# Kernel optimization log

Hardware: AMD Instinct MI355X
Metric: run time of the kernel (lower is better)

## Reference

```python
import jax, jax.numpy as jnp
import numpy as np

EMBED_DIM = 1024
HEADS = 16
HEAD_DIM = EMBED_DIM // HEADS


def setup_inputs() -> dict:
    key = jax.random.key(0)
    ks = jax.random.split(key, 5)
    B, N, C = 2, 2048, EMBED_DIM
    scale = 1.0 / np.sqrt(C)
    x = jax.random.normal(ks[0], (B, N, C), dtype=jnp.float32)
    W_qkv = jax.random.normal(ks[1], (C, 3 * C), dtype=jnp.float32) * scale
    b_qkv = jax.random.normal(ks[2], (3 * C,), dtype=jnp.float32) * 0.01
    W_out = jax.random.normal(ks[3], (C, C), dtype=jnp.float32) * scale
    b_out = jax.random.normal(ks[4], (C,), dtype=jnp.float32) * 0.01
    return {"x": x, "W_qkv": W_qkv, "b_qkv": b_qkv, "W_out": W_out, "b_out": b_out}


def reference(x, W_qkv, b_qkv, W_out, b_out):
    B, N, C = x.shape
    qkv = x @ W_qkv + b_qkv                      # [B, N, 3C]
    qkv = qkv.reshape(B, N, 3, HEADS, HEAD_DIM)
    qkv = jnp.transpose(qkv, (2, 0, 3, 1, 4))    # [3, B, H, N, d]
    q, k, v = qkv[0], qkv[1], qkv[2]
    attn = jnp.einsum('bhnd,bhmd->bhnm', q, k) / np.sqrt(HEAD_DIM)
    attn = jax.nn.softmax(attn, axis=-1)
    out = jnp.einsum('bhnm,bhmd->bhnd', attn, v)  # [B, H, N, d]
    out = jnp.transpose(out, (0, 2, 1, 3)).reshape(B, N, C)
    return out @ W_out + b_out
```

## Files before the change

kernel.cpp:

```cpp
#include <hip/hip_runtime.h>
#include <stdint.h>

typedef __bf16 bf16_t;
typedef bf16_t bf16x8 __attribute__((ext_vector_type(8)));
typedef bf16_t bf16x2v __attribute__((ext_vector_type(2)));
typedef short short4v __attribute__((ext_vector_type(4)));
typedef float f32x4 __attribute__((ext_vector_type(4)));
typedef uint32_t u32x2 __attribute__((ext_vector_type(2)));

#define BATCH 2
#define SEQ 2048
#define CDIM 1024
#define NH 16
#define HD 64

#define QSCALE 0.18033688011f

__device__ __forceinline__ uint16_t f32_bf16(float f) {
    __bf16 h = (__bf16)f;
    return __builtin_bit_cast(uint16_t, h);
}

__device__ __forceinline__ uint32_t pack_bf16(float a, float b) {
    bf16x2v t;
    t.x = (__bf16)a;
    t.y = (__bf16)b;
    return __builtin_bit_cast(uint32_t, t);
}

__device__ __forceinline__ bf16x8 ld8(const uint16_t* p) {
    return *reinterpret_cast<const bf16x8*>(p);
}

__device__ __forceinline__ void gld16(const uint16_t* g, uint16_t* l) {
    __builtin_amdgcn_global_load_lds(
        (__attribute__((address_space(1))) void*)(g),
        (__attribute__((address_space(3))) void*)(l), 16, 0, 0);
}

#define LDS_FENCE() asm volatile("s_waitcnt lgkmcnt(0)" ::: "memory")

__global__ __launch_bounds__(256) void prep_kernel(
        const float* __restrict__ x, uint16_t* __restrict__ x_bf,
        const float* __restrict__ Wqkv, uint16_t* __restrict__ wqkvT,
        const float* __restrict__ Wout, uint16_t* __restrict__ woutT) {
    const int bid = blockIdx.x, tid = threadIdx.x;
    if (bid < 4096) {
        int i = (bid * 256 + tid) * 4;
        float4 v = *(const float4*)(x + i);
        ushort4 o;
        o.x = f32_bf16(v.x);
        o.y = f32_bf16(v.y);
        o.z = f32_bf16(v.z);
        o.w = f32_bf16(v.w);
        *(ushort4*)(x_bf + i) = o;
        return;
    }
    __shared__ float tile[32][33];
    const float* in;
    uint16_t* outp;
    int idx, Cc, ncx;
    if (bid < 4096 + 3072) { idx = bid - 4096; in = Wqkv; outp = wqkvT; Cc = 3072; ncx = 96; }
    else                   { idx = bid - 7168; in = Wout; outp = woutT; Cc = 1024; ncx = 32; }
    const int R = 1024;
    int bx = idx % ncx, by = idx / ncx;
    int c0 = bx * 32, r0 = by * 32;
    int tx = tid & 31, ty = tid >> 5;
#pragma unroll
    for (int i = 0; i < 4; i++)
        tile[ty + i * 8][tx] = in[(size_t)(r0 + ty + i * 8) * Cc + c0 + tx];
    __syncthreads();
#pragma unroll
    for (int i = 0; i < 4; i++) {
        int rr = ty + i * 8;
        outp[(size_t)(c0 + rr) * R + r0 + tx] = f32_bf16(tile[tx][rr]);
    }
}

template <int BM, int BN, int MODE>
__global__ __launch_bounds__(256) void gemm_t(
        const uint16_t* __restrict__ A, const uint16_t* __restrict__ Bt, int K,
        const float* __restrict__ bias,
        uint16_t* __restrict__ qw, uint16_t* __restrict__ kw, uint16_t* __restrict__ vt,
        float* __restrict__ out) {
    constexpr int WT_M = BM / 2, WT_N = BN / 2;
    constexpr int MI = WT_M / 16, NJ = WT_N / 16;
    constexpr int ASEG_W = BM / 64, BSEG_W = BN / 64;
    constexpr int AB = 2 * BM * 32 + 2 * BN * 32;
    constexpr int TS = (MODE == 0) ? 4 * 64 * 68 : 0;
    constexpr int SM = AB > TS ? AB : TS;
    __shared__ uint16_t smem[SM];
    uint16_t* As = smem;
    uint16_t* Bs = smem + 2 * BM * 32;

    const int m0 = blockIdx.y * BM, n0 = blockIdx.x * BN;
    const int tid = threadIdx.x;
    const int w = tid >> 6, lane = tid & 63;
    const int quad = lane >> 4, l16 = lane & 15;
    const int wm = (w >> 1) * WT_M, wn = (w & 1) * WT_N;

    const int srow = lane >> 2;
    const int schunk = (lane & 3) ^ (srow & 3);

    const uint16_t* aP[ASEG_W];
    const uint16_t* bP[BSEG_W];
    int aL[ASEG_W], bL[BSEG_W];
#pragma unroll
    for (int s = 0; s < ASEG_W; s++) {
        int seg = w * ASEG_W + s;
        aP[s] = A + (size_t)(m0 + seg * 16 + srow) * K + schunk * 8;
        aL[s] = seg * 512;
    }
#pragma unroll
    for (int s = 0; s < BSEG_W; s++) {
        int seg = w * BSEG_W + s;
        bP[s] = Bt + (size_t)(n0 + seg * 16 + srow) * K + schunk * 8;
        bL[s] = seg * 512;
    }

    auto stage = [&](int buf, int k0) {
#pragma unroll
        for (int s = 0; s < ASEG_W; s++) gld16(aP[s] + k0, As + buf * BM * 32 + aL[s]);
#pragma unroll
        for (int s = 0; s < BSEG_W; s++) gld16(bP[s] + k0, Bs + buf * BN * 32 + bL[s]);
    };

    const int cslot = (quad ^ (l16 & 3)) * 8;
    f32x4 acc[MI][NJ] = {};

    stage(0, 0);
    const int iters = K / 32;
    for (int it = 0; it < iters; ++it) {
        __syncthreads();
        if (it + 1 < iters) stage((it + 1) & 1, (it + 1) * 32);
        const uint16_t* A_ = As + (it & 1) * BM * 32;
        const uint16_t* B_ = Bs + (it & 1) * BN * 32;
        bf16x8 af[MI], bfr[NJ];
#pragma unroll
        for (int i = 0; i < MI; i++) af[i] = ld8(&A_[(wm + i * 16 + l16) * 32 + cslot]);
#pragma unroll
        for (int j = 0; j < NJ; j++) bfr[j] = ld8(&B_[(wn + j * 16 + l16) * 32 + cslot]);
#pragma unroll
        for (int i = 0; i < MI; i++)
#pragma unroll
            for (int j = 0; j < NJ; j++)
                acc[i][j] = __builtin_amdgcn_mfma_f32_16x16x32_bf16(af[i], bfr[j], acc[i][j], 0, 0, 0);
    }

    const int nbase = n0 + wn;
    float bj[NJ];
#pragma unroll
    for (int j = 0; j < NJ; j++) bj[j] = bias[nbase + j * 16 + l16];

    if constexpr (MODE == 1) {
#pragma unroll
        for (int j = 0; j < NJ; j++) {
#pragma unroll
            for (int i = 0; i < MI; i++)
#pragma unroll
                for (int r = 0; r < 4; r++) {
                    int m = m0 + wm + i * 16 + quad * 4 + r;
                    out[(size_t)m * CDIM + nbase + j * 16 + l16] = acc[i][j][r] + bj[j];
                }
        }
    } else {
        __syncthreads();
        uint16_t* T = smem + w * 64 * 68;
        const int gmb = m0 + wm;
        const int b = gmb >> 11, ns0 = gmb & 2047;

        if (nbase < 2048) {
            const int which = nbase >> 10, h = (nbase & 1023) >> 6;
            const float sc = (which == 0) ? QSCALE : 1.0f;
#pragma unroll
            for (int i = 0; i < 4; i++)
#pragma unroll
                for (int j = 0; j < 4; j++)
#pragma unroll
                    for (int r = 0; r < 4; r++)
                        T[(i * 16 + quad * 4 + r) * 68 + j * 16 + l16] =
                            f32_bf16((acc[i][j][r] + bj[j]) * sc);
            LDS_FENCE();
            uint16_t* dst = ((which == 0) ? qw : kw) +
                            (((size_t)b * NH + h) * SEQ + ns0 + lane) * HD;
#pragma unroll
            for (int g = 0; g < 8; g++) {
                bf16x8 v = ld8(&T[lane * 68 + g * 8]);
                *(bf16x8*)(dst + g * 8) = v;
            }
        } else {
#pragma unroll
            for (int i = 0; i < 4; i++)
#pragma unroll
                for (int j = 0; j < 4; j++) {
                    u32x2 pr;
                    pr.x = pack_bf16(acc[i][j][0] + bj[j], acc[i][j][1] + bj[j]);
                    pr.y = pack_bf16(acc[i][j][2] + bj[j], acc[i][j][3] + bj[j]);
                    *(u32x2*)&T[(j * 16 + l16) * 68 + i * 16 + quad * 4] = pr;
                }
            LDS_FENCE();
            const int h = (nbase - 2048) >> 6;
            uint16_t* dst = vt + (((size_t)b * NH + h) * HD + lane) * SEQ + ns0;
#pragma unroll
            for (int g = 0; g < 16; g++) {
                u32x2 d2 = *(const u32x2*)&T[lane * 68 + g * 4];
                int npos = (g & 3) * 16 + (g >> 2) * 4;
                *(u32x2*)(dst + npos) = d2;
            }
        }
    }
}

__global__ __launch_bounds__(256) void attn_kernel(
        const uint16_t* __restrict__ qg, const uint16_t* __restrict__ kg,
        const uint16_t* __restrict__ vt, uint16_t* __restrict__ og) {
    __shared__ uint16_t Ks[2][64 * 64];
    __shared__ uint16_t Vs[2][64 * 64];

    const int bh = blockIdx.x;
    const int qt = blockIdx.y;
    const int tid = threadIdx.x;
    const int w = tid >> 6, lane = tid & 63;
    const int quad = lane >> 4, l16 = lane & 15;
    const int qrow0 = qt * 128 + w * 32;
    const size_t base = (size_t)bh * SEQ * HD;

    bf16x8 qf[2][2];
#pragma unroll
    for (int mg = 0; mg < 2; mg++)
#pragma unroll
        for (int ks = 0; ks < 2; ks++)
            qf[mg][ks] = ld8(qg + base + (size_t)(qrow0 + mg * 16 + l16) * HD + ks * 32 + quad * 8);

    const int srow = lane >> 3;
    const int schunk = (lane & 7) ^ srow;
    const int seg0 = w * 2, seg1 = seg0 + 1;
    const uint16_t* ksrc0 = kg + base + (size_t)(seg0 * 8 + srow) * HD + schunk * 8;
    const uint16_t* ksrc1 = kg + base + (size_t)(seg1 * 8 + srow) * HD + schunk * 8;
    const uint16_t* vsrc0 = vt + base + (size_t)(seg0 * 8 + srow) * SEQ + schunk * 8;
    const uint16_t* vsrc1 = vt + base + (size_t)(seg1 * 8 + srow) * SEQ + schunk * 8;
    const int soff0 = seg0 * 512, soff1 = seg1 * 512;

    f32x4 o_acc[2][4] = {};
    f32x4 l_acc[2] = {};
    const short4v ones = { (short)0x3F80, (short)0x3F80, (short)0x3F80, (short)0x3F80 };

    gld16(ksrc0, &Ks[0][soff0]); gld16(ksrc1, &Ks[0][soff1]);
    gld16(vsrc0, &Vs[0][soff0]); gld16(vsrc1, &Vs[0][soff1]);
    ksrc0 += 64 * HD; ksrc1 += 64 * HD; vsrc0 += 64; vsrc1 += 64;

    for (int it = 0; it < SEQ / 64; ++it) {
        __syncthreads();
        if (it + 1 < SEQ / 64) {
            int pb = (it + 1) & 1;
            gld16(ksrc0, &Ks[pb][soff0]); gld16(ksrc1, &Ks[pb][soff1]);
            gld16(vsrc0, &Vs[pb][soff0]); gld16(vsrc1, &Vs[pb][soff1]);
            ksrc0 += 64 * HD; ksrc1 += 64 * HD; vsrc0 += 64; vsrc1 += 64;
        }
        const uint16_t* K_ = Ks[it & 1];
        const uint16_t* V_ = Vs[it & 1];

        f32x4 S[2][4] = {};
#pragma unroll
        for (int nf = 0; nf < 4; nf++) {
#pragma unroll
            for (int ks = 0; ks < 2; ks++) {
                bf16x8 kf = ld8(&K_[(nf * 16 + l16) * 64 + (((ks * 4 + quad) ^ (l16 & 7)) * 8)]);
#pragma unroll
                for (int mg = 0; mg < 2; mg++)
                    S[mg][nf] = __builtin_amdgcn_mfma_f32_16x16x32_bf16(kf, qf[mg][ks], S[mg][nf], 0, 0, 0);
            }
        }

        uint32_t pk[2][4][2];
#pragma unroll
        for (int mg = 0; mg < 2; mg++)
#pragma unroll
            for (int nf = 0; nf < 4; nf++) {
                float p0 = __builtin_amdgcn_exp2f(S[mg][nf][0]);
                float p1 = __builtin_amdgcn_exp2f(S[mg][nf][1]);
                float p2 = __builtin_amdgcn_exp2f(S[mg][nf][2]);
                float p3 = __builtin_amdgcn_exp2f(S[mg][nf][3]);
                pk[mg][nf][0] = pack_bf16(p0, p1);
                pk[mg][nf][1] = pack_bf16(p2, p3);
            }

#pragma unroll
        for (int mg = 0; mg < 2; mg++)
#pragma unroll
            for (int kc = 0; kc < 4; kc++) {
                short4v pfrag = __builtin_bit_cast(short4v, (u32x2){pk[mg][kc][0], pk[mg][kc][1]});
                l_acc[mg] = __builtin_amdgcn_mfma_f32_16x16x16bf16_1k(ones, pfrag, l_acc[mg], 0, 0, 0);
            }

#pragma unroll
        for (int mf = 0; mf < 4; mf++) {
            const int ro = (mf * 16 + l16) * 64;
            uint4 v0 = *(const uint4*)&V_[ro + (((quad * 2 + 0) ^ (l16 & 7)) * 8)];
            uint4 v1 = *(const uint4*)&V_[ro + (((quad * 2 + 1) ^ (l16 & 7)) * 8)];
            short4v vf[4];
            vf[0] = __builtin_bit_cast(short4v, (u32x2){v0.x, v0.y});
            vf[1] = __builtin_bit_cast(short4v, (u32x2){v0.z, v0.w});
            vf[2] = __builtin_bit_cast(short4v, (u32x2){v1.x, v1.y});
            vf[3] = __builtin_bit_cast(short4v, (u32x2){v1.z, v1.w});
#pragma unroll
            for (int kc = 0; kc < 4; kc++)
#pragma unroll
                for (int mg = 0; mg < 2; mg++) {
                    short4v pfrag = __builtin_bit_cast(short4v, (u32x2){pk[mg][kc][0], pk[mg][kc][1]});
                    o_acc[mg][mf] = __builtin_amdgcn_mfma_f32_16x16x16bf16_1k(vf[kc], pfrag, o_acc[mg][mf], 0, 0, 0);
                }
        }
    }

    const int b = bh >> 4, h = bh & 15;
#pragma unroll
    for (int mg = 0; mg < 2; mg++) {
        const float inv = __builtin_amdgcn_rcpf(l_acc[mg][0]);
        const int ns = qrow0 + mg * 16 + l16;
        uint16_t* orow = og + (((size_t)b * SEQ + ns) * NH + h) * HD + quad * 4;
#pragma unroll
        for (int mf = 0; mf < 4; mf++) {
            ushort4 o;
            o.x = f32_bf16(o_acc[mg][mf][0] * inv);
            o.y = f32_bf16(o_acc[mg][mf][1] * inv);
            o.z = f32_bf16(o_acc[mg][mf][2] * inv);
            o.w = f32_bf16(o_acc[mg][mf][3] * inv);
            *(ushort4*)(orow + mf * 16) = o;
        }
    }
}

extern "C" void kernel_launch(void* const* d_in, const int* in_sizes, int n_in,
                              void* d_out, int out_size, void* d_ws, size_t ws_size,
                              hipStream_t stream) {
    const float* x = (const float*)d_in[0];
    const float* Wqkv = (const float*)d_in[1];
    const float* bqkv = (const float*)d_in[2];
    const float* Wout = (const float*)d_in[3];
    const float* bout = (const float*)d_in[4];
    float* out = (float*)d_out;

    uint16_t* ws = (uint16_t*)d_ws;
    uint16_t* x_bf  = ws;
    uint16_t* wqkvT = x_bf + 4194304;
    uint16_t* woutT = wqkvT + 3145728;
    uint16_t* qw    = woutT + 1048576;
    uint16_t* kw    = qw + 4194304;
    uint16_t* vtw   = kw + 4194304;
    uint16_t* attn  = vtw + 4194304;

    prep_kernel<<<8192, 256, 0, stream>>>(x, x_bf, Wqkv, wqkvT, Wout, woutT);

    gemm_t<128, 128, 0><<<dim3(24, 32), 256, 0, stream>>>(
        x_bf, wqkvT, 1024, bqkv, qw, kw, vtw, nullptr);

    attn_kernel<<<dim3(32, 16), 256, 0, stream>>>(qw, kw, vtw, attn);

    gemm_t<64, 128, 1><<<dim3(8, 64), 256, 0, stream>>>(
        attn, woutT, 1024, bout, nullptr, nullptr, nullptr, out);
}
```

Before: 189.8 us.

## Load K/V fragments directly from global memory, drop LDS staging and MFMA row-sum

Removes the shared-memory double buffers and __syncthreads in the attention kernel, so each wave reads its K and V MFMA fragments straight from global memory (relying on L1/L2 for reuse across the four waves). The loop processes 128 keys per iteration in two 64-key sub-steps, and V loads are issued ahead of the QK MFMAs. The softmax denominator is now accumulated with scalar adds and reduced with cross-lane shuffles at the end, replacing the ones-vector MFMA. This drops block-level synchronisation and LDS traffic but adds redundant global/cache loads per wave and more register pressure.

```diff
diff --git a/kernel.cpp b/kernel.cpp
--- a/kernel.cpp
+++ b/kernel.cpp
@@ -214,9 +214,6 @@
 __global__ __launch_bounds__(256) void attn_kernel(
         const uint16_t* __restrict__ qg, const uint16_t* __restrict__ kg,
         const uint16_t* __restrict__ vt, uint16_t* __restrict__ og) {
-    __shared__ uint16_t Ks[2][64 * 64];
-    __shared__ uint16_t Vs[2][64 * 64];
-
     const int bh = blockIdx.x;
     const int qt = blockIdx.y;
     const int tid = threadIdx.x;
@@ -232,91 +229,82 @@
         for (int ks = 0; ks < 2; ks++)
             qf[mg][ks] = ld8(qg + base + (size_t)(qrow0 + mg * 16 + l16) * HD + ks * 32 + quad * 8);
 
-    const int srow = lane >> 3;
-    const int schunk = (lane & 7) ^ srow;
-    const int seg0 = w * 2, seg1 = seg0 + 1;
-    const uint16_t* ksrc0 = kg + base + (size_t)(seg0 * 8 + srow) * HD + schunk * 8;
-    const uint16_t* ksrc1 = kg + base + (size_t)(seg1 * 8 + srow) * HD + schunk * 8;
-    const uint16_t* vsrc0 = vt + base + (size_t)(seg0 * 8 + srow) * SEQ + schunk * 8;
-    const uint16_t* vsrc1 = vt + base + (size_t)(seg1 * 8 + srow) * SEQ + schunk * 8;
-    const int soff0 = seg0 * 512, soff1 = seg1 * 512;
+    const uint16_t* kp = kg + base + (size_t)l16 * HD + quad * 8;
+    const uint16_t* vp[4];
+#pragma unroll
+    for (int mf = 0; mf < 4; mf++)
+        vp[mf] = vt + base + (size_t)(mf * 16 + l16) * SEQ + quad * 16;
 
     f32x4 o_acc[2][4] = {};
-    f32x4 l_acc[2] = {};
-    const short4v ones = { (short)0x3F80, (short)0x3F80, (short)0x3F80, (short)0x3F80 };
-
-    gld16(ksrc0, &Ks[0][soff0]); gld16(ksrc1, &Ks[0][soff1]);
-    gld16(vsrc0, &Vs[0][soff0]); gld16(vsrc1, &Vs[0][soff1]);
-    ksrc0 += 64 * HD; ksrc1 += 64 * HD; vsrc0 += 64; vsrc1 += 64;
-
-    for (int it = 0; it < SEQ / 64; ++it) {
-        __syncthreads();
-        if (it + 1 < SEQ / 64) {
-            int pb = (it + 1) & 1;
-            gld16(ksrc0, &Ks[pb][soff0]); gld16(ksrc1, &Ks[pb][soff1]);
-            gld16(vsrc0, &Vs[pb][soff0]); gld16(vsrc1, &Vs[pb][soff1]);
-            ksrc0 += 64 * HD; ksrc1 += 64 * HD; vsrc0 += 64; vsrc1 += 64;
+    float l_run[2] = {0.f, 0.f};
+
+    for (int it = 0; it < SEQ / 128; ++it) {
+#pragma unroll
+        for (int sub = 0; sub < 2; sub++) {
+            uint4 v0[4], v1[4];
+#pragma unroll
+            for (int mf = 0; mf < 4; mf++) {
+                v0[mf] = *(const uint4*)(vp[mf] + sub * 64);
+                v1[mf] = *(const uint4*)(vp[mf] + sub * 64 + 8);
+            }
+
+            f32x4 S[2][4] = {};
+#pragma unroll
+            for (int nf = 0; nf < 4; nf++) {
+#pragma unroll
+                for (int ks = 0; ks < 2; ks++) {
+                    bf16x8 kf = ld8(kp + (size_t)(sub * 64 + nf * 16) * HD + ks * 32);
+#pragma unroll
+                    for (int mg = 0; mg < 2; mg++)
+                        S[mg][nf] = __builtin_amdgcn_mfma_f32_16x16x32_bf16(kf, qf[mg][ks], S[mg][nf], 0, 0, 0);
+                }
+            }
+
+            uint32_t pk[2][4][2];
+#pragma unroll
+            for (int mg = 0; mg < 2; mg++) {
+                float rs = 0.f;
+#pragma unroll
+                for (int nf = 0; nf < 4; nf++) {
+                    float p0 = __builtin_amdgcn_exp2f(S[mg][nf][0]);
+                    float p1 = __builtin_amdgcn_exp2f(S[mg][nf][1]);
+                    float p2 = __builtin_amdgcn_exp2f(S[mg][nf][2]);
+                    float p3 = __builtin_amdgcn_exp2f(S[mg][nf][3]);
+                    rs += (p0 + p1) + (p2 + p3);
+                    pk[mg][nf][0] = pack_bf16(p0, p1);
+                    pk[mg][nf][1] = pack_bf16(p2, p3);
+                }
+                l_run[mg] += rs;
+            }
+
+#pragma unroll
+            for (int mf = 0; mf < 4; mf++) {
+                short4v vf[4];
+                vf[0] = __builtin_bit_cast(short4v, (u32x2){v0[mf].x, v0[mf].y});
+                vf[1] = __builtin_bit_cast(short4v, (u32x2){v0[mf].z, v0[mf].w});
+                vf[2] = __builtin_bit_cast(short4v, (u32x2){v1[mf].x, v1[mf].y});
+                vf[3] = __builtin_bit_cast(short4v, (u32x2){v1[mf].z, v1[mf].w});
+#pragma unroll
+                for (int kc = 0; kc < 4; kc++)
+#pragma unroll
+                    for (int mg = 0; mg < 2; mg++) {
+                        short4v pfrag = __builtin_bit_cast(short4v, (u32x2){pk[mg][kc][0], pk[mg][kc][1]});
+                        o_acc[mg][mf] = __builtin_amdgcn_mfma_f32_16x16x16bf16_1k(vf[kc], pfrag, o_acc[mg][mf], 0, 0, 0);
+                    }
+            }
         }
-        const uint16_t* K_ = Ks[it & 1];
-        const uint16_t* V_ = Vs[it & 1];
-
-        f32x4 S[2][4] = {};
-#pragma unroll
-        for (int nf = 0; nf < 4; nf++) {
-#pragma unroll
-            for (int ks = 0; ks < 2; ks++) {
-                bf16x8 kf = ld8(&K_[(nf * 16 + l16) * 64 + (((ks * 4 + quad) ^ (l16 & 7)) * 8)]);
-#pragma unroll
-                for (int mg = 0; mg < 2; mg++)
-                    S[mg][nf] = __builtin_amdgcn_mfma_f32_16x16x32_bf16(kf, qf[mg][ks], S[mg][nf], 0, 0, 0);
-            }
-        }
-
-        uint32_t pk[2][4][2];
-#pragma unroll
-        for (int mg = 0; mg < 2; mg++)
-#pragma unroll
-            for (int nf = 0; nf < 4; nf++) {
-                float p0 = __builtin_amdgcn_exp2f(S[mg][nf][0]);
-                float p1 = __builtin_amdgcn_exp2f(S[mg][nf][1]);
-                float p2 = __builtin_amdgcn_exp2f(S[mg][nf][2]);
-                float p3 = __builtin_amdgcn_exp2f(S[mg][nf][3]);
-                pk[mg][nf][0] = pack_bf16(p0, p1);
-                pk[mg][nf][1] = pack_bf16(p2, p3);
-            }
-
-#pragma unroll
-        for (int mg = 0; mg < 2; mg++)
-#pragma unroll
-            for (int kc = 0; kc < 4; kc++) {
-                short4v pfrag = __builtin_bit_cast(short4v, (u32x2){pk[mg][kc][0], pk[mg][kc][1]});
-                l_acc[mg] = __builtin_amdgcn_mfma_f32_16x16x16bf16_1k(ones, pfrag, l_acc[mg], 0, 0, 0);
-            }
-
-#pragma unroll
-        for (int mf = 0; mf < 4; mf++) {
-            const int ro = (mf * 16 + l16) * 64;
-            uint4 v0 = *(const uint4*)&V_[ro + (((quad * 2 + 0) ^ (l16 & 7)) * 8)];
-            uint4 v1 = *(const uint4*)&V_[ro + (((quad * 2 + 1) ^ (l16 & 7)) * 8)];
-            short4v vf[4];
-            vf[0] = __builtin_bit_cast(short4v, (u32x2){v0.x, v0.y});
-            vf[1] = __builtin_bit_cast(short4v, (u32x2){v0.z, v0.w});
-            vf[2] = __builtin_bit_cast(short4v, (u32x2){v1.x, v1.y});
-            vf[3] = __builtin_bit_cast(short4v, (u32x2){v1.z, v1.w});
-#pragma unroll
-            for (int kc = 0; kc < 4; kc++)
-#pragma unroll
-                for (int mg = 0; mg < 2; mg++) {
-                    short4v pfrag = __builtin_bit_cast(short4v, (u32x2){pk[mg][kc][0], pk[mg][kc][1]});
-                    o_acc[mg][mf] = __builtin_amdgcn_mfma_f32_16x16x16bf16_1k(vf[kc], pfrag, o_acc[mg][mf], 0, 0, 0);
-                }
-        }
+        kp += 128 * HD;
+#pragma unroll
+        for (int mf = 0; mf < 4; mf++) vp[mf] += 128;
     }
 
     const int b = bh >> 4, h = bh & 15;
 #pragma unroll
     for (int mg = 0; mg < 2; mg++) {
-        const float inv = __builtin_amdgcn_rcpf(l_acc[mg][0]);
+        float l = l_run[mg];
+        l += __shfl_xor(l, 16);
+        l += __shfl_xor(l, 32);
+        const float inv = __builtin_amdgcn_rcpf(l);
         const int ns = qrow0 + mg * 16 + l16;
         uint16_t* orow = og + (((size_t)b * SEQ + ns) * NH + h) * HD + quad * 4;
 #pragma unroll
```

Result: slower. 253.7 us (+33.7%).
